# Performance work log

Measured on AMD Instinct MI355X. Metric: run time of the kernel, lower is better.

## Reference

```python
import jax, jax.numpy as jnp
import numpy as np

B, T, C = 2, 2048, 2048
H, HKV, D = 16, 4, 128
GROUPS = H // HKV  # num_key_value_groups
EPS = 1e-6


def setup_inputs() -> dict:
    key = jax.random.key(0)
    ks = jax.random.split(key, 6)
    s = 0.02
    return {
        "hidden_states": jax.random.normal(ks[0], (B, T, C), jnp.float32),
        "Wq": jax.random.normal(ks[1], (C, H * D), jnp.float32) * s,
        "Wk": jax.random.normal(ks[2], (C, HKV * D), jnp.float32) * s,
        "Wv": jax.random.normal(ks[3], (C, HKV * D), jnp.float32) * s,
        "Wo": jax.random.normal(ks[4], (H * D, C), jnp.float32) * s,
        "keep_mask": jax.random.randint(ks[5], (T,), 0, 2) > 0,
    }


def reference(hidden_states, Wq, Wk, Wv, Wo, keep_mask):
    # Base attention (standard causal GQA attention with output_attentions=True)
    q = (hidden_states @ Wq).reshape(B, T, H, D).transpose(0, 2, 1, 3)      # [B,H,T,D]
    k = (hidden_states @ Wk).reshape(B, T, HKV, D).transpose(0, 2, 1, 3)    # [B,Hkv,S,D]
    v = (hidden_states @ Wv).reshape(B, T, HKV, D).transpose(0, 2, 1, 3)    # [B,Hkv,S,D]
    k_rep = jnp.repeat(k, GROUPS, axis=1)                                    # [B,H,S,D]
    v_rep = jnp.repeat(v, GROUPS, axis=1)                                    # [B,H,S,D]
    scale = 1.0 / jnp.sqrt(jnp.float32(D))
    scores = jnp.einsum("bhtd,bhsd->bhts", q, k_rep) * scale                 # [B,H,T,S]
    causal = jnp.tril(jnp.ones((T, T), dtype=bool))
    scores = jnp.where(causal[None, None], scores, jnp.float32(-1e9))
    attn_w = jax.nn.softmax(scores, axis=-1)                                 # [B,H,T,S]

    # ScratchpadPrunedAttention: mask dropped positions, renormalize,
    # recompute context and o_proj.
    keep = keep_mask.astype(attn_w.dtype)[None, None, None, :]               # [1,1,1,S]
    attn_w = attn_w * keep
    attn_w = attn_w / (attn_w.sum(-1, keepdims=True) + EPS)
    new_ctx = jnp.einsum("bhts,bhsd->bhtd", attn_w, v_rep)                   # [B,H,T,D]
    new_ctx = new_ctx.transpose(0, 2, 1, 3).reshape(B, T, H * D)             # [B,T,H*D]
    out = new_ctx @ Wo                                                        # [B,T,C]
    return out, attn_w
```

## Files before the change

### kernel.cpp

```cpp
#include <hip/hip_runtime.h>
#include <hip/hip_bf16.h>
#include <stdint.h>

#define B_ 2
#define T_ 2048
#define C_ 2048
#define H_ 16
#define HKV_ 4
#define D_ 128
#define M_ (B_*T_)
static constexpr float SCL = 0.08838834764831845f * 1.4426950408889634f;
static constexpr float EPS_ = 1e-6f;

typedef short bf16x8 __attribute__((ext_vector_type(8)));
typedef float f32x4 __attribute__((ext_vector_type(4)));

__device__ __forceinline__ f32x4 zero4() {
  f32x4 v; v[0] = 0.f; v[1] = 0.f; v[2] = 0.f; v[3] = 0.f; return v;
}

__device__ __forceinline__ unsigned short f2bf(float x) {
  union { __bf16 h; unsigned short u; } v;
  v.h = (__bf16)x;
  return v.u;
}

__device__ __forceinline__ void gl_lds16(const void* g, void* l) {
  __builtin_amdgcn_global_load_lds((const __attribute__((address_space(1))) void*)g,
                                   (__attribute__((address_space(3))) void*)l, 16, 0, 0);
}

__global__ void k_cvt(const float* __restrict__ in, unsigned short* __restrict__ out, int n) {
  int i = (blockIdx.x * blockDim.x + threadIdx.x) * 8;
  int stride = gridDim.x * blockDim.x * 8;
  for (; i < n; i += stride) {
    float4 a = *(const float4*)(in + i);
    float4 b = *(const float4*)(in + i + 4);
    ushort4 o0; o0.x = f2bf(a.x); o0.y = f2bf(a.y); o0.z = f2bf(a.z); o0.w = f2bf(a.w);
    ushort4 o1; o1.x = f2bf(b.x); o1.y = f2bf(b.y); o1.z = f2bf(b.z); o1.w = f2bf(b.w);
    *(ushort4*)(out + i) = o0;
    *(ushort4*)(out + i + 4) = o1;
  }
}

__global__ void k_cvt_t(const float* __restrict__ in, unsigned short* __restrict__ out,
                        int R, int Cc) {
  __shared__ float ld[32][33];
  int c0 = blockIdx.x * 32, r0 = blockIdx.y * 32;
  int x = threadIdx.x, y = threadIdx.y;
#pragma unroll
  for (int i = 0; i < 4; i++)
    ld[y * 4 + i][x] = in[(size_t)(r0 + y * 4 + i) * Cc + c0 + x];
  __syncthreads();
#pragma unroll
  for (int i = 0; i < 4; i++)
    out[(size_t)(c0 + y * 4 + i) * R + r0 + x] = f2bf(ld[x][y * 4 + i]);
}

__global__ void k_maskbits(const int* __restrict__ mask, unsigned int* __restrict__ mb) {
  int t = threadIdx.x;
  if (t < 64) {
    unsigned int w = 0;
    for (int b = 0; b < 32; b++)
      if (mask[t * 32 + b] != 0) w |= (1u << b);
    mb[t] = w;
  }
}

template <int WRITE_F32>
__global__ __launch_bounds__(256) void k_gemm(const unsigned short* __restrict__ A,
                                              const unsigned short* __restrict__ Bt,
                                              void* __restrict__ Cout,
                                              int Mdim, int Ndim, int K) {
  __shared__ __align__(16) unsigned short As[128 * 64];
  __shared__ __align__(16) unsigned short Bs[128 * 64];
  const int tid = threadIdx.x;
  const int wid = tid >> 6, lane = tid & 63;
  const int wm = wid >> 1, wn = wid & 1;
  const int m0 = blockIdx.y * 128, n0 = blockIdx.x * 128;
  const int lrow = tid >> 3, lcol = (tid & 7) * 8;
  const int g = lane >> 4, lr = lane & 15;

  f32x4 acc[4][4];
#pragma unroll
  for (int i = 0; i < 4; i++)
#pragma unroll
    for (int j = 0; j < 4; j++) acc[i][j] = zero4();

  for (int k0 = 0; k0 < K; k0 += 64) {
    __syncthreads();
#pragma unroll
    for (int it = 0; it < 4; it++) {
      gl_lds16(A + (size_t)(m0 + lrow + it * 32) * K + k0 + lcol, (void*)(As + tid * 8 + it * 2048));
      gl_lds16(Bt + (size_t)(n0 + lrow + it * 32) * K + k0 + lcol, (void*)(Bs + tid * 8 + it * 2048));
    }
    __syncthreads();
#pragma unroll
    for (int kk = 0; kk < 2; kk++) {
      bf16x8 af[4], bfr[4];
#pragma unroll
      for (int i = 0; i < 4; i++)
        af[i] = *(const bf16x8*)(As + (wm * 64 + i * 16 + lr) * 64 + kk * 32 + g * 8);
#pragma unroll
      for (int j = 0; j < 4; j++)
        bfr[j] = *(const bf16x8*)(Bs + (wn * 64 + j * 16 + lr) * 64 + kk * 32 + g * 8);
#pragma unroll
      for (int i = 0; i < 4; i++)
#pragma unroll
        for (int j = 0; j < 4; j++)
          acc[i][j] = __builtin_amdgcn_mfma_f32_16x16x32_bf16(af[i], bfr[j], acc[i][j], 0, 0, 0);
    }
  }

#pragma unroll
  for (int i = 0; i < 4; i++)
#pragma unroll
    for (int j = 0; j < 4; j++)
#pragma unroll
      for (int r = 0; r < 4; r++) {
        int row = m0 + wm * 64 + i * 16 + g * 4 + r;
        int col = n0 + wn * 64 + j * 16 + lr;
        if (WRITE_F32)
          ((float*)Cout)[(size_t)row * Ndim + col] = acc[i][j][r];
        else
          ((unsigned short*)Cout)[(size_t)row * Ndim + col] = f2bf(acc[i][j][r]);
      }
}

__global__ __launch_bounds__(256, 4) void k_attn(const unsigned short* __restrict__ qb,
                                                 const unsigned short* __restrict__ kb,
                                                 const unsigned short* __restrict__ vt,
                                                 const unsigned int* __restrict__ mb,
                                                 float* __restrict__ attn,
                                                 unsigned short* __restrict__ ctx)
{
  __shared__ __align__(16) unsigned short KV[128 * 128];
  __shared__ __align__(16) unsigned short Ps[4][16 * 64];
  unsigned short* Ks = KV;
  unsigned short* Vs = KV + 64 * 128;

  const int tid = threadIdx.x;
  const int wid = tid >> 6, lane = tid & 63;
  const int g = lane >> 4, lr = lane & 15;
  const int lr7 = lr & 7;
  const int qt = 31 - blockIdx.y;
  const int bh = blockIdx.x;
  const int b = bh >> 4, h = bh & 15, hkv = h >> 2;
  const int qbase = qt * 64;

  const unsigned short* qp = qb + (size_t)(b * T_ + qbase) * 2048 + h * 128;
  const unsigned short* kp = kb + (size_t)(b * T_) * 512 + hkv * 128;
  const unsigned short* vp = vt + (size_t)(hkv * 128) * 4096 + b * T_;
  float* ap = attn + (size_t)(bh * T_ + qbase) * 2048;
  unsigned short* cp = ctx + (size_t)(b * T_ + qbase) * 2048 + h * 128;

  bf16x8 qa[4];
#pragma unroll
  for (int ks = 0; ks < 4; ks++)
    qa[ks] = *(const bf16x8*)(qp + (size_t)(wid * 16 + lr) * 2048 + ks * 32 + g * 8);

  const int srow = tid >> 4;
  const int scolb = ((tid & 15) * 16) ^ ((srow & 7) << 4);
  const int vrow = tid >> 3;
  const int vcolb = ((tid & 7) * 16) ^ ((vrow & 7) << 4);

  float z[4] = {0, 0, 0, 0}, zk[4] = {0, 0, 0, 0};

  const int ntile1 = (qt >> 1) + 1;
  for (int st = 0; st < ntile1; st++) {
    __syncthreads();
    {
      const unsigned short* src = kp + (size_t)(st * 128 + srow) * 512 + (scolb >> 1);
      unsigned short* dst = KV + tid * 8;
#pragma unroll
      for (int it = 0; it < 8; it++)
        gl_lds16(src + (size_t)it * 16 * 512, (void*)(dst + it * 2048));
    }
    __syncthreads();
    const int dj = qbase + wid * 16 - st * 128;
    int jcut = (dj + 1) >> 4; jcut = jcut < 0 ? 0 : (jcut > 8 ? 8 : jcut);
    int jend = ((dj + 15) >> 4) + 1; jend = jend < jcut ? jcut : (jend > 8 ? 8 : jend);
    for (int j = 0; j < jcut; j++) {
      f32x4 sc = zero4();
      const unsigned short* kbase = KV + (j * 16 + lr) * 128;
#pragma unroll
      for (int ks = 0; ks < 4; ks++) {
        bf16x8 kf = *(const bf16x8*)(kbase + (((ks * 64 + g * 16) ^ (lr7 << 4)) >> 1));
        sc = __builtin_amdgcn_mfma_f32_16x16x32_bf16(qa[ks], kf, sc, 0, 0, 0);
      }
      unsigned int w = mb[st * 4 + (j >> 1)];
      float kpv = (float)((w >> ((j & 1) * 16 + lr)) & 1u);
#pragma unroll
      for (int r = 0; r < 4; r++) {
        float e = __builtin_amdgcn_exp2f(sc[r] * SCL);
        z[r] += e;
        zk[r] += e * kpv;
      }
    }
    for (int j = jcut; j < jend; j++) {
      f32x4 sc = zero4();
      const unsigned short* kbase = KV + (j * 16 + lr) * 128;
#pragma unroll
      for (int ks = 0; ks < 4; ks++) {
        bf16x8 kf = *(const bf16x8*)(kbase + (((ks * 64 + g * 16) ^ (lr7 << 4)) >> 1));
        sc = __builtin_amdgcn_mfma_f32_16x16x32_bf16(qa[ks], kf, sc, 0, 0, 0);
      }
      int sg = st * 128 + j * 16 + lr;
      unsigned int w = mb[st * 4 + (j >> 1)];
      float kpv = (float)((w >> ((j & 1) * 16 + lr)) & 1u);
#pragma unroll
      for (int r = 0; r < 4; r++) {
        int tg = qbase + wid * 16 + g * 4 + r;
        float e = (sg <= tg) ? __builtin_amdgcn_exp2f(sc[r] * SCL) : 0.0f;
        z[r] += e;
        zk[r] += e * kpv;
      }
    }
  }
#pragma unroll
  for (int r = 0; r < 4; r++) {
#pragma unroll
    for (int m = 1; m < 16; m <<= 1) {
      z[r] += __shfl_xor(z[r], m);
      zk[r] += __shfl_xor(zk[r], m);
    }
  }
  float inv[4];
#pragma unroll
  for (int r = 0; r < 4; r++) inv[r] = 1.0f / (zk[r] + EPS_ * z[r]);

  f32x4 cacc[8];
#pragma unroll
  for (int n = 0; n < 8; n++) cacc[n] = zero4();

  for (int st = qt; st >= 0; st--) {
    __syncthreads();
    {
      const unsigned short* srcK = kp + (size_t)(st * 64 + srow) * 512 + (scolb >> 1);
      const unsigned short* srcV = vp + (size_t)vrow * 4096 + st * 64 + (vcolb >> 1);
      unsigned short* dstK = Ks + tid * 8;
      unsigned short* dstV = Vs + tid * 8;
#pragma unroll
      for (int it = 0; it < 4; it++) {
        gl_lds16(srcK + (size_t)it * 16 * 512, (void*)(dstK + it * 2048));
        gl_lds16(srcV + (size_t)it * 32 * 4096, (void*)(dstV + it * 2048));
      }
    }
    __syncthreads();
    const int s0 = st * 64;
    const bool diag = (st == qt);
#pragma unroll
    for (int j = 0; j < 4; j++) {
      f32x4 sc = zero4();
      const unsigned short* kbase = Ks + (j * 16 + lr) * 128;
#pragma unroll
      for (int ks = 0; ks < 4; ks++) {
        bf16x8 kf = *(const bf16x8*)(kbase + (((ks * 64 + g * 16) ^ (lr7 << 4)) >> 1));
        sc = __builtin_amdgcn_mfma_f32_16x16x32_bf16(qa[ks], kf, sc, 0, 0, 0);
      }
      int sg = s0 + j * 16 + lr;
      unsigned int w = mb[st * 2 + (j >> 1)];
      float kpv = (float)((w >> ((j & 1) * 16 + lr)) & 1u);
      if (diag) {
#pragma unroll
        for (int r = 0; r < 4; r++) {
          int row = wid * 16 + g * 4 + r;
          int tg = qbase + row;
          float e = (sg <= tg) ? __builtin_amdgcn_exp2f(sc[r] * SCL) : 0.0f;
          float a = e * kpv * inv[r];
          ap[(size_t)row * 2048 + sg] = a;
          int prow = g * 4 + r;
          Ps[wid][prow * 64 + (((j * 32 + lr * 2) ^ ((prow & 7) << 4)) >> 1)] = f2bf(a);
        }
      } else {
#pragma unroll
        for (int r = 0; r < 4; r++) {
          int row = wid * 16 + g * 4 + r;
          float e = __builtin_amdgcn_exp2f(sc[r] * SCL);
          float a = e * kpv * inv[r];
          ap[(size_t)row * 2048 + sg] = a;
          int prow = g * 4 + r;
          Ps[wid][prow * 64 + (((j * 32 + lr * 2) ^ ((prow & 7) << 4)) >> 1)] = f2bf(a);
        }
      }
    }
    asm volatile("s_waitcnt lgkmcnt(0)" ::: "memory");
    __builtin_amdgcn_sched_barrier(0);
#pragma unroll
    for (int kk = 0; kk < 2; kk++) {
      bf16x8 pa = *(const bf16x8*)(&Ps[wid][lr * 64 + (((kk * 64 + g * 16) ^ (lr7 << 4)) >> 1)]);
#pragma unroll
      for (int n = 0; n < 8; n++) {
        int vrw = n * 16 + lr;
        bf16x8 vf = *(const bf16x8*)(Vs + vrw * 64 + (((kk * 64 + g * 16) ^ ((vrw & 7) << 4)) >> 1));
        cacc[n] = __builtin_amdgcn_mfma_f32_16x16x32_bf16(pa, vf, cacc[n], 0, 0, 0);
      }
    }
  }

#pragma unroll
  for (int n = 0; n < 8; n++)
#pragma unroll
    for (int r = 0; r < 4; r++)
      cp[(size_t)(wid * 16 + g * 4 + r) * 2048 + n * 16 + lr] = f2bf(cacc[n][r]);

  const int zc0 = qbase + 64;
  if (zc0 < 2048) {
    float4 zf; zf.x = 0.f; zf.y = 0.f; zf.z = 0.f; zf.w = 0.f;
    float* aprow = ap + (size_t)(tid >> 2) * 2048;
    for (int c = zc0 + (tid & 3) * 4; c < 2048; c += 16)
      *(float4*)(aprow + c) = zf;
  }
}

extern "C" void kernel_launch(void* const* d_in, const int* in_sizes, int n_in,
                              void* d_out, int out_size, void* d_ws, size_t ws_size,
                              hipStream_t stream) {
  const float* hs = (const float*)d_in[0];
  const float* Wq = (const float*)d_in[1];
  const float* Wk = (const float*)d_in[2];
  const float* Wv = (const float*)d_in[3];
  const float* Wo = (const float*)d_in[4];
  const int* mask = (const int*)d_in[5];

  char* w = (char*)d_ws;
  unsigned short* hsb = (unsigned short*)w; w += (size_t)M_ * C_ * 2;
  unsigned short* Wqt = (unsigned short*)w; w += (size_t)2048 * 2048 * 2;
  unsigned short* Wkt = (unsigned short*)w; w += (size_t)512 * 2048 * 2;
  unsigned short* Wvt = (unsigned short*)w; w += (size_t)512 * 2048 * 2;
  unsigned short* Wot = (unsigned short*)w; w += (size_t)2048 * 2048 * 2;
  unsigned short* qbuf = (unsigned short*)w; w += (size_t)M_ * 2048 * 2;
  unsigned short* kbuf = (unsigned short*)w; w += (size_t)M_ * 512 * 2;
  unsigned short* vtb = (unsigned short*)w; w += (size_t)512 * M_ * 2;
  unsigned short* ctxb = (unsigned short*)w; w += (size_t)M_ * 2048 * 2;
  unsigned int* mbits = (unsigned int*)w;  w += 256;

  float* out = (float*)d_out;
  float* attn = out + (size_t)M_ * C_;

  k_cvt<<<2048, 256, 0, stream>>>(hs, hsb, M_ * C_);
  k_cvt_t<<<dim3(2048 / 32, 2048 / 32), dim3(32, 8), 0, stream>>>(Wq, Wqt, 2048, 2048);
  k_cvt_t<<<dim3(512 / 32, 2048 / 32), dim3(32, 8), 0, stream>>>(Wk, Wkt, 2048, 512);
  k_cvt_t<<<dim3(512 / 32, 2048 / 32), dim3(32, 8), 0, stream>>>(Wv, Wvt, 2048, 512);
  k_cvt_t<<<dim3(2048 / 32, 2048 / 32), dim3(32, 8), 0, stream>>>(Wo, Wot, 2048, 2048);
  k_maskbits<<<1, 64, 0, stream>>>(mask, mbits);

  k_gemm<0><<<dim3(2048 / 128, 4096 / 128), 256, 0, stream>>>(hsb, Wqt, qbuf, 4096, 2048, 2048);
  k_gemm<0><<<dim3(512 / 128, 4096 / 128), 256, 0, stream>>>(hsb, Wkt, kbuf, 4096, 512, 2048);
  k_gemm<0><<<dim3(4096 / 128, 512 / 128), 256, 0, stream>>>(Wvt, hsb, vtb, 512, 4096, 2048);

  k_attn<<<dim3(32, 32), 256, 0, stream>>>(qbuf, kbuf, vtb, mbits, attn, ctxb);

  k_gemm<1><<<dim3(2048 / 128, 4096 / 128), 256, 0, stream>>>(ctxb, Wot, out, 4096, 2048, 2048);
}
```

Measured before the change: 456.7 us.

## Load K and V fragments directly from global memory instead of LDS staging

Drops the shared-memory K/V tiles and the block-wide barriers in both attention passes. Each wave now reads its MFMA operand fragments for K and transposed V straight from global memory, relying on L1/L2 caching. The first (normalizer) pass also switches from 128-wide to 64-wide key tiles with a separate diagonal tile. This frees LDS and removes synchronisation, but gives up cross-wave reuse of K/V and issues more, narrower global loads per wave.

```diff
diff --git a/kernel.cpp b/kernel.cpp
--- a/kernel.cpp
+++ b/kernel.cpp
@@ -134,10 +134,7 @@
                                                  float* __restrict__ attn,
                                                  unsigned short* __restrict__ ctx)
 {
-  __shared__ __align__(16) unsigned short KV[128 * 128];
   __shared__ __align__(16) unsigned short Ps[4][16 * 64];
-  unsigned short* Ks = KV;
-  unsigned short* Vs = KV + 64 * 128;
 
   const int tid = threadIdx.x;
   const int wid = tid >> 6, lane = tid & 63;
@@ -149,7 +146,7 @@
   const int qbase = qt * 64;
 
   const unsigned short* qp = qb + (size_t)(b * T_ + qbase) * 2048 + h * 128;
-  const unsigned short* kp = kb + (size_t)(b * T_) * 512 + hkv * 128;
+  const unsigned short* kp = kb + (size_t)(b * T_) * 512 + hkv * 128 + g * 8;
   const unsigned short* vp = vt + (size_t)(hkv * 128) * 4096 + b * T_;
   float* ap = attn + (size_t)(bh * T_ + qbase) * 2048;
   unsigned short* cp = ctx + (size_t)(b * T_ + qbase) * 2048 + h * 128;
@@ -159,36 +156,23 @@
   for (int ks = 0; ks < 4; ks++)
     qa[ks] = *(const bf16x8*)(qp + (size_t)(wid * 16 + lr) * 2048 + ks * 32 + g * 8);
 
-  const int srow = tid >> 4;
-  const int scolb = ((tid & 15) * 16) ^ ((srow & 7) << 4);
-  const int vrow = tid >> 3;
-  const int vcolb = ((tid & 7) * 16) ^ ((vrow & 7) << 4);
-
   float z[4] = {0, 0, 0, 0}, zk[4] = {0, 0, 0, 0};
 
-  const int ntile1 = (qt >> 1) + 1;
-  for (int st = 0; st < ntile1; st++) {
-    __syncthreads();
-    {
-      const unsigned short* src = kp + (size_t)(st * 128 + srow) * 512 + (scolb >> 1);
-      unsigned short* dst = KV + tid * 8;
-#pragma unroll
-      for (int it = 0; it < 8; it++)
-        gl_lds16(src + (size_t)it * 16 * 512, (void*)(dst + it * 2048));
-    }
-    __syncthreads();
-    const int dj = qbase + wid * 16 - st * 128;
-    int jcut = (dj + 1) >> 4; jcut = jcut < 0 ? 0 : (jcut > 8 ? 8 : jcut);
-    int jend = ((dj + 15) >> 4) + 1; jend = jend < jcut ? jcut : (jend > 8 ? 8 : jend);
-    for (int j = 0; j < jcut; j++) {
+  for (int st = 0; st < qt; st++) {
+    const int s0 = st * 64;
+#pragma unroll
+    for (int j = 0; j < 4; j++) {
+      const unsigned short* kr = kp + (size_t)(s0 + j * 16 + lr) * 512;
+      bf16x8 k0 = *(const bf16x8*)(kr);
+      bf16x8 k1 = *(const bf16x8*)(kr + 32);
+      bf16x8 k2 = *(const bf16x8*)(kr + 64);
+      bf16x8 k3 = *(const bf16x8*)(kr + 96);
       f32x4 sc = zero4();
-      const unsigned short* kbase = KV + (j * 16 + lr) * 128;
-#pragma unroll
-      for (int ks = 0; ks < 4; ks++) {
-        bf16x8 kf = *(const bf16x8*)(kbase + (((ks * 64 + g * 16) ^ (lr7 << 4)) >> 1));
-        sc = __builtin_amdgcn_mfma_f32_16x16x32_bf16(qa[ks], kf, sc, 0, 0, 0);
-      }
-      unsigned int w = mb[st * 4 + (j >> 1)];
+      sc = __builtin_amdgcn_mfma_f32_16x16x32_bf16(qa[0], k0, sc, 0, 0, 0);
+      sc = __builtin_amdgcn_mfma_f32_16x16x32_bf16(qa[1], k1, sc, 0, 0, 0);
+      sc = __builtin_amdgcn_mfma_f32_16x16x32_bf16(qa[2], k2, sc, 0, 0, 0);
+      sc = __builtin_amdgcn_mfma_f32_16x16x32_bf16(qa[3], k3, sc, 0, 0, 0);
+      unsigned int w = mb[st * 2 + (j >> 1)];
       float kpv = (float)((w >> ((j & 1) * 16 + lr)) & 1u);
 #pragma unroll
       for (int r = 0; r < 4; r++) {
@@ -197,16 +181,23 @@
         zk[r] += e * kpv;
       }
     }
-    for (int j = jcut; j < jend; j++) {
+  }
+  {
+    const int s0 = qt * 64;
+#pragma unroll
+    for (int j = 0; j < 4; j++) {
+      const unsigned short* kr = kp + (size_t)(s0 + j * 16 + lr) * 512;
+      bf16x8 k0 = *(const bf16x8*)(kr);
+      bf16x8 k1 = *(const bf16x8*)(kr + 32);
+      bf16x8 k2 = *(const bf16x8*)(kr + 64);
+      bf16x8 k3 = *(const bf16x8*)(kr + 96);
       f32x4 sc = zero4();
-      const unsigned short* kbase = KV + (j * 16 + lr) * 128;
-#pragma unroll
-      for (int ks = 0; ks < 4; ks++) {
-        bf16x8 kf = *(const bf16x8*)(kbase + (((ks * 64 + g * 16) ^ (lr7 << 4)) >> 1));
-        sc = __builtin_amdgcn_mfma_f32_16x16x32_bf16(qa[ks], kf, sc, 0, 0, 0);
-      }
-      int sg = st * 128 + j * 16 + lr;
-      unsigned int w = mb[st * 4 + (j >> 1)];
+      sc = __builtin_amdgcn_mfma_f32_16x16x32_bf16(qa[0], k0, sc, 0, 0, 0);
+      sc = __builtin_amdgcn_mfma_f32_16x16x32_bf16(qa[1], k1, sc, 0, 0, 0);
+      sc = __builtin_amdgcn_mfma_f32_16x16x32_bf16(qa[2], k2, sc, 0, 0, 0);
+      sc = __builtin_amdgcn_mfma_f32_16x16x32_bf16(qa[3], k3, sc, 0, 0, 0);
+      int sg = s0 + j * 16 + lr;
+      unsigned int w = mb[qt * 2 + (j >> 1)];
       float kpv = (float)((w >> ((j & 1) * 16 + lr)) & 1u);
 #pragma unroll
       for (int r = 0; r < 4; r++) {
@@ -234,30 +225,20 @@
   for (int n = 0; n < 8; n++) cacc[n] = zero4();
 
   for (int st = qt; st >= 0; st--) {
-    __syncthreads();
-    {
-      const unsigned short* srcK = kp + (size_t)(st * 64 + srow) * 512 + (scolb >> 1);
-      const unsigned short* srcV = vp + (size_t)vrow * 4096 + st * 64 + (vcolb >> 1);
-      unsigned short* dstK = Ks + tid * 8;
-      unsigned short* dstV = Vs + tid * 8;
-#pragma unroll
-      for (int it = 0; it < 4; it++) {
-        gl_lds16(srcK + (size_t)it * 16 * 512, (void*)(dstK + it * 2048));
-        gl_lds16(srcV + (size_t)it * 32 * 4096, (void*)(dstV + it * 2048));
-      }
-    }
-    __syncthreads();
     const int s0 = st * 64;
     const bool diag = (st == qt);
 #pragma unroll
     for (int j = 0; j < 4; j++) {
+      const unsigned short* kr = kp + (size_t)(s0 + j * 16 + lr) * 512;
+      bf16x8 k0 = *(const bf16x8*)(kr);
+      bf16x8 k1 = *(const bf16x8*)(kr + 32);
+      bf16x8 k2 = *(const bf16x8*)(kr + 64);
+      bf16x8 k3 = *(const bf16x8*)(kr + 96);
       f32x4 sc = zero4();
-      const unsigned short* kbase = Ks + (j * 16 + lr) * 128;
-#pragma unroll
-      for (int ks = 0; ks < 4; ks++) {
-        bf16x8 kf = *(const bf16x8*)(kbase + (((ks * 64 + g * 16) ^ (lr7 << 4)) >> 1));
-        sc = __builtin_amdgcn_mfma_f32_16x16x32_bf16(qa[ks], kf, sc, 0, 0, 0);
-      }
+      sc = __builtin_amdgcn_mfma_f32_16x16x32_bf16(qa[0], k0, sc, 0, 0, 0);
+      sc = __builtin_amdgcn_mfma_f32_16x16x32_bf16(qa[1], k1, sc, 0, 0, 0);
+      sc = __builtin_amdgcn_mfma_f32_16x16x32_bf16(qa[2], k2, sc, 0, 0, 0);
+      sc = __builtin_amdgcn_mfma_f32_16x16x32_bf16(qa[3], k3, sc, 0, 0, 0);
       int sg = s0 + j * 16 + lr;
       unsigned int w = mb[st * 2 + (j >> 1)];
       float kpv = (float)((w >> ((j & 1) * 16 + lr)) & 1u);
@@ -289,10 +270,10 @@
 #pragma unroll
     for (int kk = 0; kk < 2; kk++) {
       bf16x8 pa = *(const bf16x8*)(&Ps[wid][lr * 64 + (((kk * 64 + g * 16) ^ (lr7 << 4)) >> 1)]);
+      const unsigned short* vb = vp + (size_t)lr * 4096 + s0 + kk * 32 + g * 8;
 #pragma unroll
       for (int n = 0; n < 8; n++) {
-        int vrw = n * 16 + lr;
-        bf16x8 vf = *(const bf16x8*)(Vs + vrw * 64 + (((kk * 64 + g * 16) ^ ((vrw & 7) << 4)) >> 1));
+        bf16x8 vf = *(const bf16x8*)(vb + (size_t)n * 16 * 4096);
         cacc[n] = __builtin_amdgcn_mfma_f32_16x16x32_bf16(pa, vf, cacc[n], 0, 0, 0);
       }
     }
```

After: 743.1 us. 1.63x slower.
